# Optimization experiments

Hardware: AMD Instinct MI355X
Metric: run time of the kernel (lower is better)

## Reference

```python
import jax, jax.numpy as jnp
import numpy as np

HIDDEN = 512
TEMPERATURE = float(np.sqrt(HIDDEN))  # scaled-dot temperature
BATCH = 64


def _build_weights(attn_weight, N, K):
    """Vectorized version of get_attn_weight: (S,S,H) with S = N*K+1.
    Regions: 0=same_sample, 1=same_class, 2=diff_class, 3=support->query,
    4=query->support, 5=query->query. Replicates the torch overwrite order."""
    S = N * K + 1
    NK = N * K
    i = jnp.arange(S)[:, None]
    j = jnp.arange(S)[None, :]
    idx = jnp.full((S, S), 2, dtype=jnp.int32)                      # w_diff_class
    idx = jnp.where((i // K) == (j // K), 1, idx)                   # w_same_class
    idx = jnp.where((i < NK) & (j == NK), 3, idx)                   # w_stoquery
    idx = jnp.where(i == j, 0, idx)                                 # w_same_sample (diag)
    idx = jnp.where((i == NK) & (j < NK), 4, idx)                   # w_querytos
    idx = jnp.where((i == NK) & (j == NK), 5, idx)                  # w_query
    return attn_weight[idx]  # (S, S, H)


def setup_inputs() -> dict:
    key = jax.random.key(0)
    kq, kk, kv, kw = jax.random.split(key, 4)
    N, K = 10, 10
    S = N * K + 1  # 101
    q = jax.random.normal(kq, (BATCH, S, HIDDEN), dtype=jnp.float32)
    k = jax.random.normal(kk, (BATCH, S, HIDDEN), dtype=jnp.float32)
    v = jax.random.normal(kv, (BATCH, S, HIDDEN), dtype=jnp.float32)
    bound = float(np.sqrt(6 / 2))
    attn_weight = jax.random.uniform(kw, (6, HIDDEN), dtype=jnp.float32,
                                     minval=-bound, maxval=bound)
    return {"q": q, "k": k, "v": v, "attn_weight": attn_weight, "N": N, "K": K}


def reference(q, k, v, attn_weight, N, K):
    # attn[b,i,j] = softmax_j(q.k^T / temperature)
    scores = jnp.einsum("bih,bjh->bij", q, k) / TEMPERATURE
    attn = jax.nn.softmax(scores, axis=2)  # dropout p=0 (eval) -> identity
    weights = _build_weights(attn_weight, N, K)  # (S,S,H)
    # out[b,i,h] = sum_j attn[b,i,j] * weights[i,j,h] * v[b,j,h]
    out = jnp.einsum("bij,ijh,bjh->bih", attn, weights, v)
    return out, attn
```

## Files before the change

### kernel.cpp

```cpp
#include <hip/hip_runtime.h>
#include <math.h>
#include <stdint.h>

#define BATCH 64
#define SEQ   101
#define HID   512
#define NKQ   100
#define KCLS  10
#define INV_TEMP 0.04419417382415922f

typedef short bf16x8 __attribute__((ext_vector_type(8)));
typedef float f32x4  __attribute__((ext_vector_type(4)));
typedef uint32_t u32x4 __attribute__((ext_vector_type(4)));

__device__ inline uint32_t cvt2(float a, float b) {
    uint32_t r;
    asm("v_cvt_pk_bf16_f32 %0, %1, %2" : "=v"(r) : "v"(a), "v"(b));
    return r;
}
__device__ inline void split_bf16(float x, short& hi, short& lo) {
    uint32_t u = __builtin_bit_cast(uint32_t, x);
    hi = (short)(u >> 16);
    float hf = __builtin_bit_cast(float, u & 0xFFFF0000u);
    float l  = x - hf;
    lo = (short)(__builtin_bit_cast(uint32_t, l) >> 16);
}

#define QST 520

#define OFF_QLO 16640
#define POOLSZ  33280

__global__ __launch_bounds__(512, 4)
void fused_attn(const float* __restrict__ q, const float* __restrict__ k,
                const float* __restrict__ v, const float* __restrict__ aw,
                float* __restrict__ out, float* __restrict__ attn) {
    __shared__ __align__(16) char pool[POOLSZ];
    __shared__ __align__(16) float sc[16][132];
    short (*qhi)[QST] = (short(*)[QST])(pool);
    short (*qlo)[QST] = (short(*)[QST])(pool + OFF_QLO);

    const int b   = blockIdx.x & 63;
    const int i0  = (blockIdx.x >> 6) * 16;
    const int tid = threadIdx.x;
    const int wv  = tid >> 6, lane = tid & 63;
    const int m   = lane & 15;
    const int g   = lane >> 4;
    const int kq  = g * 8;
    const int rq  = g * 4;
    const int j0w = wv * 16;

    const float* qb = q + (size_t)b * SEQ * HID;
    const float* kb = k + (size_t)b * SEQ * HID;
    const float* vb = v + (size_t)b * SEQ * HID;

    #pragma unroll
    for (int s = 0; s < 4; ++s) {
        const int f = tid + s * 512;
        const int r = f >> 7, c = (f & 127) << 2;
        const int gi = i0 + r;
        f32x4 x = {};
        if (gi < SEQ) x = *(const f32x4*)(qb + (size_t)gi * HID + c);
        short4 hv, lv;
        split_bf16(x[0], hv.x, lv.x);
        split_bf16(x[1], hv.y, lv.y);
        split_bf16(x[2], hv.z, lv.z);
        split_bf16(x[3], hv.w, lv.w);
        *(short4*)&qhi[r][c] = hv;
        *(short4*)&qlo[r][c] = lv;
    }
    __syncthreads();

    f32x4 acc = {};
    {
        const int jg = j0w + m;
        const int jr = (jg > NKQ) ? NKQ : jg;
        const float* kr = kb + (size_t)jr * HID + kq;
        f32x4 k0 = *(const f32x4*)(kr);
        f32x4 k1 = *(const f32x4*)(kr + 4);
        #pragma unroll
        for (int ks = 0; ks < 16; ++ks) {
            f32x4 n0 = {}, n1 = {};
            if (ks < 15) {
                n0 = *(const f32x4*)(kr + (ks + 1) * 32);
                n1 = *(const f32x4*)(kr + (ks + 1) * 32 + 4);
            }
            u32x4 kp;
            kp[0] = cvt2(k0[0], k0[1]); kp[1] = cvt2(k0[2], k0[3]);
            kp[2] = cvt2(k1[0], k1[1]); kp[3] = cvt2(k1[2], k1[3]);
            const bf16x8 kH = __builtin_bit_cast(bf16x8, kp);
            const bf16x8 qH = *(const bf16x8*)&qhi[m][ks * 32 + kq];
            const bf16x8 qL = *(const bf16x8*)&qlo[m][ks * 32 + kq];
            acc = __builtin_amdgcn_mfma_f32_16x16x32_bf16(qH, kH, acc, 0, 0, 0);
            acc = __builtin_amdgcn_mfma_f32_16x16x32_bf16(qL, kH, acc, 0, 0, 0);
            k0 = n0; k1 = n1;
        }
    }
    #pragma unroll
    for (int r = 0; r < 4; ++r)
        sc[rq + r][j0w + m] = acc[r];
    __syncthreads();

    {
        const int row = tid >> 5, t32 = tid & 31;
        const int gi  = i0 + row;
        float mx = -1e30f;
        for (int j = t32; j < SEQ; j += 32) {
            float s = sc[row][j] * INV_TEMP;
            sc[row][j] = s;
            mx = fmaxf(mx, s);
        }
        #pragma unroll
        for (int off = 1; off < 32; off <<= 1) mx = fmaxf(mx, __shfl_xor(mx, off));
        float sum = 0.f;
        for (int j = t32; j < SEQ; j += 32) {
            float e = __expf(sc[row][j] - mx);
            sc[row][j] = e;
            sum += e;
        }
        #pragma unroll
        for (int off = 1; off < 32; off <<= 1) sum += __shfl_xor(sum, off);
        const float inv = 1.f / sum;
        float* arow = attn + ((size_t)b * SEQ + gi) * SEQ;
        for (int j = t32; j < SEQ; j += 32) {
            float a = sc[row][j] * inv;
            sc[row][j] = a;
            if (gi < SEQ) arow[j] = a;
        }
        for (int j = SEQ + t32; j < 128; j += 32) sc[row][j] = 0.f;
    }
    __syncthreads();

    int ai = i0 + m; if (ai > NKQ) ai = NKQ;
    const int ci = ai / KCLS;
    uint32_t mbits = 0;
    #pragma unroll
    for (int ks = 0; ks < 4; ++ks)
        #pragma unroll
        for (int e = 0; e < 8; ++e)
            if (((ks * 32 + kq + e) / KCLS) == ci) mbits |= (1u << (ks * 8 + e));
    bf16x8 Ah[4], Al[4];
    #pragma unroll
    for (int ks = 0; ks < 4; ++ks) {
        const f32x4 u0 = *(const f32x4*)&sc[m][ks * 32 + kq];
        const f32x4 u1 = *(const f32x4*)&sc[m][ks * 32 + kq + 4];
        const float x[8] = {u0[0], u0[1], u0[2], u0[3], u1[0], u1[1], u1[2], u1[3]};
        #pragma unroll
        for (int e = 0; e < 8; ++e) {
            short h, l; split_bf16(x[e], h, l);
            Ah[ks][e] = h; Al[ks][e] = l;
        }
    }

    const int hl = j0w + m;
    for (int hc = 0; hc < 4; ++hc) {
        const int h = (hc << 7) + hl;
        const float* vh = vb + h;
        f32x4 T = {}, U = {};
        #pragma unroll
        for (int ks = 0; ks < 4; ++ks) {
            float xv[8];
            #pragma unroll
            for (int e = 0; e < 8; ++e) {
                const int j  = ks * 32 + kq + e;
                const int jr = (j > NKQ) ? NKQ : j;
                xv[e] = vh[(size_t)jr * HID];
            }
            u32x4 ph, pl;
            #pragma unroll
            for (int p = 0; p < 4; ++p) {
                const uint32_t h01 = cvt2(xv[2 * p], xv[2 * p + 1]);
                const float r0 = xv[2 * p]     - __builtin_bit_cast(float, h01 << 16);
                const float r1 = xv[2 * p + 1] - __builtin_bit_cast(float, h01 & 0xFFFF0000u);
                ph[p] = h01;
                pl[p] = cvt2(r0, r1);
            }
            const bf16x8 Bh = __builtin_bit_cast(bf16x8, ph);
            const bf16x8 Bl = __builtin_bit_cast(bf16x8, pl);
            bf16x8 Mh;
            #pragma unroll
            for (int e = 0; e < 8; ++e)
                Mh[e] = (mbits & (1u << (ks * 8 + e))) ? Ah[ks][e] : (short)0;
            T = __builtin_amdgcn_mfma_f32_16x16x32_bf16(Ah[ks], Bh, T, 0, 0, 0);
            T = __builtin_amdgcn_mfma_f32_16x16x32_bf16(Ah[ks], Bl, T, 0, 0, 0);
            T = __builtin_amdgcn_mfma_f32_16x16x32_bf16(Al[ks], Bh, T, 0, 0, 0);
            U = __builtin_amdgcn_mfma_f32_16x16x32_bf16(Mh,     Bh, U, 0, 0, 0);
        }
        const float w0 = aw[0 * HID + h], w1 = aw[1 * HID + h], w2 = aw[2 * HID + h];
        const float w3 = aw[3 * HID + h], w4 = aw[4 * HID + h], w5 = aw[5 * HID + h];
        const float vN = vb[(size_t)NKQ * HID + h];
        #pragma unroll
        for (int r = 0; r < 4; ++r) {
            const int i = i0 + rq + r;
            if (i >= SEQ) continue;
            const int il = rq + r;
            const float t = T[r], u = U[r];
            const float aiN = sc[il][NKQ];
            float o;
            if (i < NKQ) {
                const float aii = sc[il][i];
                const float vi  = vb[(size_t)i * HID + h];
                o = w2 * t + (w1 - w2) * u + (w0 - w1) * aii * vi + (w3 - w2) * aiN * vN;
            } else {
                o = w4 * t + (w5 - w4) * aiN * vN;
            }
            out[((size_t)b * SEQ + i) * HID + h] = o;
        }
    }
}

extern "C" void kernel_launch(void* const* d_in, const int* in_sizes, int n_in,
                              void* d_out, int out_size, void* d_ws, size_t ws_size,
                              hipStream_t stream) {
    const float* q  = (const float*)d_in[0];
    const float* k  = (const float*)d_in[1];
    const float* v  = (const float*)d_in[2];
    const float* aw = (const float*)d_in[3];
    float* out  = (float*)d_out;
    float* attn = out + (size_t)BATCH * SEQ * HID;
    (void)d_ws; (void)ws_size;

    fused_attn<<<dim3(448), dim3(512), 0, stream>>>(q, k, v, aw, out, attn);
}
```

Before: 111.0 us.

## Precast K to bf16 in a prep kernel and compute PV with FP32 FMAs

A separate prep kernel converts K to bf16 once into workspace, so the fused kernel loads packed bf16 K fragments directly instead of converting FP32 per block (each batch's K was converted by 7 blocks). The attention-times-V stage no longer uses split-bf16 MFMAs. It uses per-class FP32 vector FMA accumulation, where each thread handles 4 hidden columns and 4 rows and takes the same-class partial sum directly. This removes the hi/lo splitting, the masked MFMA and the redundant V conversion, at the cost of an extra launch, extra global traffic for the bf16 K copy, more scalar FMA work, and a lower occupancy hint in launch bounds.

```diff
diff --git a/kernel.cpp b/kernel.cpp
--- a/kernel.cpp
+++ b/kernel.cpp
@@ -1,4 +1,5 @@
 #include <hip/hip_runtime.h>
+#include <hip/hip_bf16.h>
 #include <math.h>
 #include <stdint.h>
 
@@ -13,9 +14,12 @@
 typedef float f32x4  __attribute__((ext_vector_type(4)));
 typedef uint32_t u32x4 __attribute__((ext_vector_type(4)));
 
+__device__ inline f32x4 vspl(float x) { return (f32x4){x, x, x, x}; }
+
 __device__ inline uint32_t cvt2(float a, float b) {
+    __hip_bfloat162 t = __float22bfloat162_rn(float2{a, b});
     uint32_t r;
-    asm("v_cvt_pk_bf16_f32 %0, %1, %2" : "=v"(r) : "v"(a), "v"(b));
+    __builtin_memcpy(&r, &t, 4);
     return r;
 }
 __device__ inline void split_bf16(float x, short& hi, short& lo) {
@@ -26,13 +30,23 @@
     lo = (short)(__builtin_bit_cast(uint32_t, l) >> 16);
 }
 
+__global__ __launch_bounds__(256)
+void prep_k(const float* __restrict__ k, uint32_t* __restrict__ kp) {
+    const int total = BATCH * SEQ * HID / 4;
+    for (int i = blockIdx.x * 256 + threadIdx.x; i < total; i += gridDim.x * 256) {
+        const f32x4 x = ((const f32x4*)k)[i];
+        kp[2 * i + 0] = cvt2(x[0], x[1]);
+        kp[2 * i + 1] = cvt2(x[2], x[3]);
+    }
+}
+
 #define QST 520
 
 #define OFF_QLO 16640
 #define POOLSZ  33280
 
-__global__ __launch_bounds__(512, 4)
-void fused_attn(const float* __restrict__ q, const float* __restrict__ k,
+__global__ __launch_bounds__(512, 2)
+void fused_attn(const float* __restrict__ q, const short* __restrict__ kp,
                 const float* __restrict__ v, const float* __restrict__ aw,
                 float* __restrict__ out, float* __restrict__ attn) {
     __shared__ __align__(16) char pool[POOLSZ];
@@ -51,7 +65,7 @@
     const int j0w = wv * 16;
 
     const float* qb = q + (size_t)b * SEQ * HID;
-    const float* kb = k + (size_t)b * SEQ * HID;
+    const short* kb = kp + (size_t)b * SEQ * HID;
     const float* vb = v + (size_t)b * SEQ * HID;
 
     #pragma unroll
@@ -75,25 +89,17 @@
     {
         const int jg = j0w + m;
         const int jr = (jg > NKQ) ? NKQ : jg;
-        const float* kr = kb + (size_t)jr * HID + kq;
-        f32x4 k0 = *(const f32x4*)(kr);
-        f32x4 k1 = *(const f32x4*)(kr + 4);
+        const short* krow = kb + (size_t)jr * HID + kq;
+        bf16x8 kf[16];
+        #pragma unroll
+        for (int ks = 0; ks < 16; ++ks)
+            kf[ks] = *(const bf16x8*)(krow + ks * 32);
         #pragma unroll
         for (int ks = 0; ks < 16; ++ks) {
-            f32x4 n0 = {}, n1 = {};
-            if (ks < 15) {
-                n0 = *(const f32x4*)(kr + (ks + 1) * 32);
-                n1 = *(const f32x4*)(kr + (ks + 1) * 32 + 4);
-            }
-            u32x4 kp;
-            kp[0] = cvt2(k0[0], k0[1]); kp[1] = cvt2(k0[2], k0[3]);
-            kp[2] = cvt2(k1[0], k1[1]); kp[3] = cvt2(k1[2], k1[3]);
-            const bf16x8 kH = __builtin_bit_cast(bf16x8, kp);
             const bf16x8 qH = *(const bf16x8*)&qhi[m][ks * 32 + kq];
             const bf16x8 qL = *(const bf16x8*)&qlo[m][ks * 32 + kq];
-            acc = __builtin_amdgcn_mfma_f32_16x16x32_bf16(qH, kH, acc, 0, 0, 0);
-            acc = __builtin_amdgcn_mfma_f32_16x16x32_bf16(qL, kH, acc, 0, 0, 0);
-            k0 = n0; k1 = n1;
+            acc = __builtin_amdgcn_mfma_f32_16x16x32_bf16(qH, kf[ks], acc, 0, 0, 0);
+            acc = __builtin_amdgcn_mfma_f32_16x16x32_bf16(qL, kf[ks], acc, 0, 0, 0);
         }
     }
     #pragma unroll
@@ -127,84 +133,69 @@
             sc[row][j] = a;
             if (gi < SEQ) arow[j] = a;
         }
-        for (int j = SEQ + t32; j < 128; j += 32) sc[row][j] = 0.f;
     }
     __syncthreads();
 
-    int ai = i0 + m; if (ai > NKQ) ai = NKQ;
-    const int ci = ai / KCLS;
-    uint32_t mbits = 0;
-    #pragma unroll
-    for (int ks = 0; ks < 4; ++ks)
-        #pragma unroll
-        for (int e = 0; e < 8; ++e)
-            if (((ks * 32 + kq + e) / KCLS) == ci) mbits |= (1u << (ks * 8 + e));
-    bf16x8 Ah[4], Al[4];
-    #pragma unroll
-    for (int ks = 0; ks < 4; ++ks) {
-        const f32x4 u0 = *(const f32x4*)&sc[m][ks * 32 + kq];
-        const f32x4 u1 = *(const f32x4*)&sc[m][ks * 32 + kq + 4];
-        const float x[8] = {u0[0], u0[1], u0[2], u0[3], u1[0], u1[1], u1[2], u1[3]};
-        #pragma unroll
-        for (int e = 0; e < 8; ++e) {
-            short h, l; split_bf16(x[e], h, l);
-            Ah[ks][e] = h; Al[ks][e] = l;
-        }
-    }
-
-    const int hl = j0w + m;
-    for (int hc = 0; hc < 4; ++hc) {
-        const int h = (hc << 7) + hl;
-        const float* vh = vb + h;
-        f32x4 T = {}, U = {};
-        #pragma unroll
-        for (int ks = 0; ks < 4; ++ks) {
-            float xv[8];
+    {
+        const int hp = tid & 127;
+        const int rg = tid >> 7;
+        const int h4 = hp << 2;
+        const float* vcol = vb + h4;
+
+        int cir[4];
+        #pragma unroll
+        for (int rr = 0; rr < 4; ++rr)
+            cir[rr] = (i0 + rg * 4 + rr) / KCLS;
+
+        f32x4 accT[4] = {}, accU[4] = {};
+        #pragma unroll 1
+        for (int cls = 0; cls < 10; ++cls) {
+            f32x4 seg[4] = {};
+            const int jb = cls * KCLS;
+            #pragma unroll 5
+            for (int t = 0; t < KCLS; ++t) {
+                const int j = jb + t;
+                const f32x4 vj = *(const f32x4*)(vcol + (size_t)j * HID);
+                #pragma unroll
+                for (int rr = 0; rr < 4; ++rr) {
+                    const float p = sc[rg * 4 + rr][j];
+                    seg[rr] += vspl(p) * vj;
+                }
+            }
             #pragma unroll
-            for (int e = 0; e < 8; ++e) {
-                const int j  = ks * 32 + kq + e;
-                const int jr = (j > NKQ) ? NKQ : j;
-                xv[e] = vh[(size_t)jr * HID];
+            for (int rr = 0; rr < 4; ++rr) {
+                accT[rr] += seg[rr];
+                if (cls == cir[rr]) accU[rr] = seg[rr];
             }
-            u32x4 ph, pl;
-            #pragma unroll
-            for (int p = 0; p < 4; ++p) {
-                const uint32_t h01 = cvt2(xv[2 * p], xv[2 * p + 1]);
-                const float r0 = xv[2 * p]     - __builtin_bit_cast(float, h01 << 16);
-                const float r1 = xv[2 * p + 1] - __builtin_bit_cast(float, h01 & 0xFFFF0000u);
-                ph[p] = h01;
-                pl[p] = cvt2(r0, r1);
-            }
-            const bf16x8 Bh = __builtin_bit_cast(bf16x8, ph);
-            const bf16x8 Bl = __builtin_bit_cast(bf16x8, pl);
-            bf16x8 Mh;
-            #pragma unroll
-            for (int e = 0; e < 8; ++e)
-                Mh[e] = (mbits & (1u << (ks * 8 + e))) ? Ah[ks][e] : (short)0;
-            T = __builtin_amdgcn_mfma_f32_16x16x32_bf16(Ah[ks], Bh, T, 0, 0, 0);
-            T = __builtin_amdgcn_mfma_f32_16x16x32_bf16(Ah[ks], Bl, T, 0, 0, 0);
-            T = __builtin_amdgcn_mfma_f32_16x16x32_bf16(Al[ks], Bh, T, 0, 0, 0);
-            U = __builtin_amdgcn_mfma_f32_16x16x32_bf16(Mh,     Bh, U, 0, 0, 0);
-        }
-        const float w0 = aw[0 * HID + h], w1 = aw[1 * HID + h], w2 = aw[2 * HID + h];
-        const float w3 = aw[3 * HID + h], w4 = aw[4 * HID + h], w5 = aw[5 * HID + h];
-        const float vN = vb[(size_t)NKQ * HID + h];
-        #pragma unroll
-        for (int r = 0; r < 4; ++r) {
-            const int i = i0 + rq + r;
+        }
+        const f32x4 vN4 = *(const f32x4*)(vcol + (size_t)NKQ * HID);
+        #pragma unroll
+        for (int rr = 0; rr < 4; ++rr)
+            accT[rr] += vspl(sc[rg * 4 + rr][NKQ]) * vN4;
+
+        const f32x4 w0 = *(const f32x4*)(aw + 0 * HID + h4);
+        const f32x4 w1 = *(const f32x4*)(aw + 1 * HID + h4);
+        const f32x4 w2 = *(const f32x4*)(aw + 2 * HID + h4);
+        const f32x4 w3 = *(const f32x4*)(aw + 3 * HID + h4);
+        const f32x4 w4 = *(const f32x4*)(aw + 4 * HID + h4);
+        const f32x4 w5 = *(const f32x4*)(aw + 5 * HID + h4);
+        #pragma unroll
+        for (int rr = 0; rr < 4; ++rr) {
+            const int il = rg * 4 + rr;
+            const int i  = i0 + il;
             if (i >= SEQ) continue;
-            const int il = rq + r;
-            const float t = T[r], u = U[r];
             const float aiN = sc[il][NKQ];
-            float o;
+            f32x4 o;
             if (i < NKQ) {
                 const float aii = sc[il][i];
-                const float vi  = vb[(size_t)i * HID + h];
-                o = w2 * t + (w1 - w2) * u + (w0 - w1) * aii * vi + (w3 - w2) * aiN * vN;
+                const f32x4 vi  = *(const f32x4*)(vcol + (size_t)i * HID);
+                o = w2 * accT[rr] + (w1 - w2) * accU[rr]
+                  + (w0 - w1) * vspl(aii) * vi
+                  + (w3 - w2) * vspl(aiN) * vN4;
             } else {
-                o = w4 * t + (w5 - w4) * aiN * vN;
+                o = w4 * accT[rr] + (w5 - w4) * vspl(aiN) * vN4;
             }
-            out[((size_t)b * SEQ + i) * HID + h] = o;
+            *(f32x4*)(out + ((size_t)b * SEQ + i) * HID + h4) = o;
         }
     }
 }
@@ -218,7 +209,9 @@
     const float* aw = (const float*)d_in[3];
     float* out  = (float*)d_out;
     float* attn = out + (size_t)BATCH * SEQ * HID;
-    (void)d_ws; (void)ws_size;
-
-    fused_attn<<<dim3(448), dim3(512), 0, stream>>>(q, k, v, aw, out, attn);
-}
+    uint32_t* kp = (uint32_t*)d_ws;
+
+    prep_k<<<dim3(512), dim3(256), 0, stream>>>(k, kp);
+    fused_attn<<<dim3(448), dim3(512), 0, stream>>>(q, (const short*)kp, v, aw,
+                                                    out, attn);
+}
```

After: 114.3 us. +3.0%, slower.
